# Kernel optimization log

Hardware: AMD Instinct MI355X
Metric: run time of the kernel (lower is better)

Reference implementation:

```python
import jax, jax.numpy as jnp
import numpy as np

DILATIONS = (1, 2, 4, 8)  # d1..d4 from init_kwargs
QUERY_C = 256
HEADS = 4


def setup_inputs() -> dict:
    key = jax.random.key(0)
    ks = jax.random.split(key, 7)
    b, c, h, w = 8, QUERY_C, 128, 128
    c4 = c // HEADS
    s1 = 1.0 / np.sqrt(c)          # kaiming-ish scale for 1x1 convs (fan_in=c)
    s3 = 1.0 / np.sqrt(c * 9)      # for 3x3 convs (fan_in=c*9)
    return {
        "query": jax.random.normal(ks[0], (b, c, h, w), dtype=jnp.float32),
        "Wq": jax.random.normal(ks[1], (HEADS, c4, c), dtype=jnp.float32) * s1,
        "bq": jax.random.normal(ks[2], (HEADS, c4), dtype=jnp.float32) * 0.01,
        "Wk": jax.random.normal(ks[3], (HEADS, c4, c, 3, 3), dtype=jnp.float32) * s3,
        "bk": jax.random.normal(ks[4], (HEADS, c4), dtype=jnp.float32) * 0.01,
        "Wv": jax.random.normal(ks[5], (HEADS, c4, c), dtype=jnp.float32) * s1,
        "bv": jax.random.normal(ks[6], (HEADS, c4), dtype=jnp.float32) * 0.01,
    }


def reference(query, Wq, bq, Wk, bk, Wv, bv):
    b, c, h, w = query.shape
    n = h * w
    c4 = c // HEADS
    xf = query.reshape(b, c, n)  # (b, c, N)

    # 1x1 conv projections for Q and V across all 4 heads at once.
    q = jnp.einsum('bcn,hoc->hbon', xf, Wq) + bq.swapaxes(0, 0)[:, None, :, None]  # (H,b,c4,N)
    v = jnp.einsum('bcn,hoc->hbon', xf, Wv) + bv[:, None, :, None]                  # (H,b,c4,N)

    # Dilated 3x3 key convs (dilation differs per head -> small fixed loop).
    keys = []
    for i, d in enumerate(DILATIONS):
        k = jax.lax.conv_general_dilated(
            query, Wk[i], window_strides=(1, 1),
            padding=[(d, d), (d, d)], rhs_dilation=(d, d),
            dimension_numbers=('NCHW', 'OIHW', 'NCHW'))
        keys.append(k.reshape(b, c4, n) + bk[i][None, :, None])
    k = jnp.stack(keys)  # (H, b, c4, N)

    # Channel attention: scores (H,b,c4,c4), contraction over N spatial tokens.
    scale = 1.0 / jnp.sqrt(jnp.asarray(c, dtype=query.dtype))
    scores = jnp.einsum('hbon,hbpn->hbop', q, k) * scale
    attn = jax.nn.softmax(scores, axis=-1)
    out = jnp.einsum('hbop,hbpn->hbon', attn, v)  # (H, b, c4, N)

    # torch: cat(split(out, 1, dim=0), dim=2).squeeze(0) -> heads concat on channel dim
    out = jnp.transpose(out, (1, 0, 2, 3)).reshape(b, c, h, w)
    return out
```

## Files before the change

kernel.cpp:

```cpp
#include <hip/hip_runtime.h>
#include <hip/hip_bf16.h>


typedef __attribute__((ext_vector_type(8))) _Float16 f16x8;
typedef __attribute__((ext_vector_type(4))) float f32x4;
typedef __attribute__((ext_vector_type(16))) float f32x16;

__device__ __forceinline__ unsigned short f2h(float f) {
  union { _Float16 h; unsigned short u; } v;
  v.h = (_Float16)f;
  return v.u;
}

__device__ __forceinline__ f32x4 mfma16(f16x8 a, f16x8 b, f32x4 c) {
  return __builtin_amdgcn_mfma_f32_16x16x32_f16(a, b, c, 0, 0, 0);
}
__device__ __forceinline__ f32x16 mfma32(f16x8 a, f16x8 b, f32x16 c) {
  return __builtin_amdgcn_mfma_f32_32x32x16_f16(a, b, c, 0, 0, 0);
}

__device__ __forceinline__ int sw(int row, int c) {
  return row * 64 + ((((c << 1) ^ ((row & 7) << 4)) >> 1));
}

__global__ __launch_bounds__(256) void prep(const float* __restrict__ Wq,
                                            const float* __restrict__ Wv,
                                            const float* __restrict__ Wk,
                                            unsigned short* __restrict__ Wqvn,
                                            unsigned short* __restrict__ Wkb,
                                            unsigned short* __restrict__ zp) {
  int i = blockIdx.x * 256 + threadIdx.x;
  if (blockIdx.x == 0) zp[threadIdx.x] = 0;
  const int total = 131072 + 589824;
  if (i >= total) return;
  if (i < 65536) {
    int jj = i & 7;
    int m31 = (i >> 3) & 31;
    int hi = (i >> 8) & 1;
    int ks = (i >> 9) & 15;
    int mt = i >> 13;
    int row = mt * 32 + m31;
    int ch = ks * 16 + hi * 8 + jj;
    Wqvn[i] = f2h(Wq[row * 256 + ch]);
  } else if (i < 131072) {
    int j2 = i - 65536;
    int p = j2 & 63;
    int c = (j2 >> 6) & 255;
    int h = j2 >> 14;
    Wqvn[i] = f2h(Wv[(size_t)(h * 64 + p) * 256 + c]);
  } else {
    int j = i - 131072;
    int jj = j & 7;
    int p = (j >> 3) & 63;
    int ks = (j >> 9) & 31;
    int ht = j >> 14;
    int t = ht % 9;
    int h = ht / 9;
    Wkb[j] = f2h(Wk[(size_t)((h * 64 + p) * 256 + ks * 8 + jj) * 9 + t]);
  }
}

__global__ __launch_bounds__(256) void xpose(const float* __restrict__ x,
                                             unsigned short* __restrict__ xT) {
  __shared__ unsigned short tile[64][66];
  int n0 = blockIdx.x * 64, c0 = blockIdx.y * 64, b = blockIdx.z;
  int t = threadIdx.x;
  int r = t >> 2, q = t & 3;
  const float* src = x + (size_t)b * 4194304 + (size_t)(c0 + r) * 16384 + n0 + q * 16;
#pragma unroll
  for (int i = 0; i < 4; i++) {
    float4 v = *(const float4*)(src + i * 4);
    tile[r][q * 16 + i * 4 + 0] = f2h(v.x);
    tile[r][q * 16 + i * 4 + 1] = f2h(v.y);
    tile[r][q * 16 + i * 4 + 2] = f2h(v.z);
    tile[r][q * 16 + i * 4 + 3] = f2h(v.w);
  }
  __syncthreads();
  int px = t & 63, s4 = t >> 6;
  unsigned short v[16];
#pragma unroll
  for (int j = 0; j < 16; j++) v[j] = tile[s4 * 16 + j][px];
  unsigned short* dst = xT + (size_t)b * 4194304 + (size_t)((c0 >> 4) + s4) * 262144 +
                        (size_t)(n0 + px) * 16;
  *(uint4*)&dst[0] = *(const uint4*)&v[0];
  *(uint4*)&dst[8] = *(const uint4*)&v[8];
}

__global__ __launch_bounds__(256) void proj(const unsigned short* __restrict__ xT,
                                            const unsigned short* __restrict__ Wqvn,
                                            const float* __restrict__ bq,
                                            unsigned short* __restrict__ qout) {
  __shared__ __align__(16) unsigned short Xs[2048 * 8];
  int n0 = blockIdx.x * 64, b = blockIdx.y;
  int tid = threadIdx.x, lane = tid & 63, w = tid >> 6;
  int l31 = lane & 31, hi = lane >> 5;
  const unsigned short* xb = xT + (size_t)b * 4194304;
#pragma unroll
  for (int it = 0; it < 8; it++) {
    int base = it * 256 + w * 64;
    int p = base + lane;
    int px = p >> 5, g = p & 31;
    int gs = g ^ (px & 31);
    const unsigned short* gsrc =
        xb + (size_t)(gs >> 1) * 262144 + (size_t)(n0 + px) * 16 + (gs & 1) * 8;
    __builtin_amdgcn_global_load_lds(
        (const __attribute__((address_space(1))) void*)gsrc,
        (__attribute__((address_space(3))) void*)&Xs[(size_t)base * 8], 16, 0, 0);
  }
  __syncthreads();

  f32x16 acc[2][2];
#pragma unroll
  for (int i = 0; i < 2; i++)
#pragma unroll
    for (int j = 0; j < 2; j++)
#pragma unroll
      for (int r = 0; r < 16; r++) acc[i][j][r] = 0.f;

#pragma unroll
  for (int ks = 0; ks < 16; ks++) {
    f16x8 bfr[2];
#pragma unroll
    for (int nt = 0; nt < 2; nt++) {
      int px = nt * 32 + l31;
      int gl = (ks * 2 + hi) ^ (px & 31);
      bfr[nt] = *(const f16x8*)&Xs[(px * 32 + gl) * 8];
    }
#pragma unroll
    for (int mj = 0; mj < 2; mj++) {
      int mt = w * 2 + mj;
      f16x8 afr = *(const f16x8*)(Wqvn + (size_t)(((mt * 16 + ks) * 2 + hi) * 32 + l31) * 8);
      acc[mj][0] = mfma32(afr, bfr[0], acc[mj][0]);
      acc[mj][1] = mfma32(afr, bfr[1], acc[mj][1]);
    }
  }

#pragma unroll
  for (int mj = 0; mj < 2; mj++) {
    int mt = w * 2 + mj;
#pragma unroll
    for (int nt = 0; nt < 2; nt++) {
      int n = n0 + nt * 32 + l31;
#pragma unroll
      for (int r = 0; r < 16; r++) {
        int og = mt * 32 + (r & 3) + 8 * (r >> 2) + 4 * hi;
        int h = og >> 6, o = og & 63;
        qout[((size_t)(h * 8 + b) * 64 + o) * 16384 + n] = f2h(acc[mj][nt][r] + bq[og]);
      }
    }
  }
}

__global__ __launch_bounds__(256, 2) void convk(const unsigned short* __restrict__ xT,
                                                const unsigned short* __restrict__ Wkb,
                                                const float* __restrict__ bk,
                                                const unsigned short* __restrict__ zp,
                                                unsigned short* __restrict__ kout) {
  __shared__ __align__(16) unsigned short Hs[2][1792 * 8];
  __shared__ __align__(16) unsigned short Ws[1280 * 8];
  int orig = (blockIdx.x & 7) * 128 + (blockIdx.x >> 3);
  int g = orig & 31, b = (orig >> 5) & 7, h = orig >> 8;
  int d = 1 << h;
  int gpd = 32 >> h;
  int s = g / gpd;
  int q0 = (g - s * gpd) * 4;
  int nq = 128 >> h;
  int tid = threadIdx.x, lane = tid & 63, w = tid >> 6;
  int l31 = lane & 31, hi = lane >> 5;
  const unsigned short* xb = xT + (size_t)b * 4194304;

  f32x16 acc[2][4];
#pragma unroll
  for (int i = 0; i < 2; i++)
#pragma unroll
    for (int j = 0; j < 4; j++)
#pragma unroll
      for (int r = 0; r < 16; r++) acc[i][j][r] = 0.f;

  const char* hptr[7];
  int hstr[7];
#pragma unroll
  for (int it = 0; it < 7; it++) {
    int p = it * 256 + tid;
    hptr[it] = (const char*)zp;
    hstr[it] = 0;
    if (p < 1728) {
      int px = p % 144;
      int sp = p / 144;
      int plane = sp % 6, slot = sp / 6;
      int q = q0 + plane - 1;
      int xc = px - d;
      bool ok = (q >= 0) & (q < nq) & (xc >= 0) & (xc < 128);
      if (ok) {
        hptr[it] = (const char*)(xb + (size_t)((s + q * d) * 128 + xc) * 16 + slot * 8);
        hstr[it] = 524288;
      }
    }
  }
  const char* wptr[5];
  int wstr[5];
#pragma unroll
  for (int it = 0; it < 5; it++) {
    int p = it * 256 + tid;
    wptr[it] = (const char*)zp;
    wstr[it] = 0;
    if (p < 1152) {
      int pp = p & 63, ts = p >> 6;
      int t = ts >> 1, slot = ts & 1;
      wptr[it] = (const char*)(Wkb + (size_t)(((h * 9 + t) * 32 + slot) * 64 + pp) * 8);
      wstr[it] = 2048;
    }
  }

  auto HSTAGE = [&](int bufi) {
#pragma unroll
    for (int it = 0; it < 7; it++) {
      int base = it * 256 + w * 64;
      __builtin_amdgcn_global_load_lds(
          (const __attribute__((address_space(1))) void*)hptr[it],
          (__attribute__((address_space(3))) void*)&Hs[bufi][(size_t)base * 8], 16, 0, 0);
      hptr[it] += hstr[it];
    }
  };
  auto WSTAGE = [&]() {
#pragma unroll
    for (int it = 0; it < 5; it++) {
      int base = it * 256 + w * 64;
      __builtin_amdgcn_global_load_lds(
          (const __attribute__((address_space(1))) void*)wptr[it],
          (__attribute__((address_space(3))) void*)&Ws[(size_t)base * 8], 16, 0, 0);
      wptr[it] += wstr[it];
    }
  };

  HSTAGE(0);
  WSTAGE();
  HSTAGE(1);
#pragma unroll 1
  for (int c = 0; c < 16; c++) {
    if (c < 15) asm volatile("s_waitcnt vmcnt(7)" ::: "memory");
    else        asm volatile("s_waitcnt vmcnt(0)" ::: "memory");
    __builtin_amdgcn_s_barrier();
    __builtin_amdgcn_sched_barrier(0);
    int bufi = c & 1;
    __builtin_amdgcn_s_setprio(1);
#pragma unroll
    for (int tx = 0; tx < 3; tx++) {
      f16x8 bfr[6];
#pragma unroll
      for (int p6 = 0; p6 < 6; p6++)
        bfr[p6] = *(const f16x8*)&Hs[bufi][((hi * 6 + p6) * 144 + w * 32 + d * tx + l31) * 8];
#pragma unroll
      for (int ty = 0; ty < 3; ty++) {
        int t = ty * 3 + tx;
        f16x8 a0 = *(const f16x8*)&Ws[((t * 2 + hi) * 64 + l31) * 8];
        f16x8 a1 = *(const f16x8*)&Ws[((t * 2 + hi) * 64 + 32 + l31) * 8];
#pragma unroll
        for (int r = 0; r < 4; r++) {
          acc[0][r] = mfma32(a0, bfr[r + ty], acc[0][r]);
          acc[1][r] = mfma32(a1, bfr[r + ty], acc[1][r]);
        }
      }
    }
    __builtin_amdgcn_s_setprio(0);
    asm volatile("s_waitcnt lgkmcnt(0)" ::: "memory");
    __builtin_amdgcn_sched_barrier(0);
    __builtin_amdgcn_s_barrier();
    __builtin_amdgcn_sched_barrier(0);
    if (c < 15) WSTAGE();
    if (c < 14) HSTAGE(bufi);
    __builtin_amdgcn_sched_barrier(0);
  }

  unsigned short* kb = kout + (size_t)((h * 8 + b) * 64) * 16384;
#pragma unroll
  for (int mo = 0; mo < 2; mo++)
#pragma unroll
    for (int r = 0; r < 4; r++) {
      int y = s + (q0 + r) * d;
#pragma unroll
      for (int reg = 0; reg < 16; reg++) {
        int p = mo * 32 + (reg & 3) + 8 * (reg >> 2) + 4 * hi;
        int x = w * 32 + l31;
        kb[(size_t)p * 16384 + y * 128 + x] = f2h(acc[mo][r][reg] + bk[h * 64 + p]);
      }
    }
}

__global__ __launch_bounds__(256) void scoresk(const unsigned short* __restrict__ qin,
                                               const unsigned short* __restrict__ kin,
                                               float* __restrict__ part) {
  __shared__ __align__(16) unsigned short As[64 * 64];
  __shared__ __align__(16) unsigned short Bs[64 * 64];
  int nch = blockIdx.x, b = blockIdx.y, h = blockIdx.z;
  int tid = threadIdx.x, lane = tid & 63, w = tid >> 6;
  int l15 = lane & 15, uq = lane >> 4;
  const unsigned short* qb = qin + (size_t)((h * 8 + b) * 64) * 16384;
  const unsigned short* kb = kin + (size_t)((h * 8 + b) * 64) * 16384;
  int moff = (w >> 1) * 32, noff = (w & 1) * 32;
  const f32x4 fz = {0.f, 0.f, 0.f, 0.f};
  f32x4 acc[2][2] = {{fz, fz}, {fz, fz}};
  const unsigned short* srcb = (w < 2) ? qb : kb;
  unsigned short* dst = (w < 2) ? As : Bs;
  int pbase = (w & 1) * 64;
  for (int ci = 0; ci < 8; ci++) {
    int nb = nch * 512 + ci * 64;
    __syncthreads();
#pragma unroll
    for (int k4 = 0; k4 < 4; k4++) {
      int p = pbase + k4 * 128 + lane;
      int row = p >> 3, j = p & 7;
      int gs = j ^ (row & 7);
      const unsigned short* gsrc = srcb + (size_t)row * 16384 + nb + gs * 8;
      __builtin_amdgcn_global_load_lds(
          (const __attribute__((address_space(1))) void*)gsrc,
          (__attribute__((address_space(3))) void*)&dst[(size_t)(pbase + k4 * 128) * 8],
          16, 0, 0);
    }
    asm volatile("s_waitcnt vmcnt(0)" ::: "memory");
    __syncthreads();
#pragma unroll
    for (int kk = 0; kk < 2; kk++) {
      f16x8 b0 = *(const f16x8*)&Bs[sw(noff + l15, kk * 32 + uq * 8)];
      f16x8 b1 = *(const f16x8*)&Bs[sw(noff + 16 + l15, kk * 32 + uq * 8)];
      f16x8 a0 = *(const f16x8*)&As[sw(moff + l15, kk * 32 + uq * 8)];
      f16x8 a1 = *(const f16x8*)&As[sw(moff + 16 + l15, kk * 32 + uq * 8)];
      acc[0][0] = mfma16(a0, b0, acc[0][0]);
      acc[0][1] = mfma16(a0, b1, acc[0][1]);
      acc[1][0] = mfma16(a1, b0, acc[1][0]);
      acc[1][1] = mfma16(a1, b1, acc[1][1]);
    }
  }
  float* pb = part + (size_t)((nch * 4 + h) * 8 + b) * 4096;
#pragma unroll
  for (int mf = 0; mf < 2; mf++)
#pragma unroll
    for (int nf = 0; nf < 2; nf++) {
      int p = noff + nf * 16 + l15;
#pragma unroll
      for (int r = 0; r < 4; r++) {
        int o = moff + mf * 16 + 4 * uq + r;
        pb[o * 64 + p] = acc[mf][nf][r];
      }
    }
}

__global__ __launch_bounds__(256) void smax(const float* __restrict__ part,
                                            const float* __restrict__ bv,
                                            unsigned short* __restrict__ attn,
                                            float* __restrict__ obias) {
  int row = blockIdx.x * 4 + (threadIdx.x >> 6);
  int lane = threadIdx.x & 63;
  int h = row >> 9, b = (row >> 6) & 7, o = row & 63;
  float s = 0.f;
#pragma unroll
  for (int nch = 0; nch < 32; nch++)
    s += part[(size_t)((nch * 4 + h) * 8 + b) * 4096 + o * 64 + lane];
  s *= 0.0625f;
  float m = s;
#pragma unroll
  for (int k = 32; k > 0; k >>= 1) m = fmaxf(m, __shfl_xor(m, k, 64));
  float e = __expf(s - m);
  float sum = e;
#pragma unroll
  for (int k = 32; k > 0; k >>= 1) sum += __shfl_xor(sum, k, 64);
  float a = e / sum;
  attn[(size_t)(h * 8 + b) * 4096 + o * 64 + lane] = f2h(a);
  float ob = a * bv[h * 64 + lane];
#pragma unroll
  for (int k = 32; k > 0; k >>= 1) ob += __shfl_xor(ob, k, 64);
  if (lane == 0) obias[b * 256 + h * 64 + o] = ob;
}

__global__ __launch_bounds__(256) void avP(const unsigned short* __restrict__ attn,
                                           const unsigned short* __restrict__ WvT,
                                           unsigned short* __restrict__ A2) {
  int b = blockIdx.x, h = blockIdx.y;
  int tid = threadIdx.x, lane = tid & 63, wq = tid >> 6;
  int l31 = lane & 31, hi = lane >> 5;
  const unsigned short* at = attn + (size_t)(h * 8 + b) * 4096;
  const unsigned short* wv = WvT + (size_t)h * 16384;
  f32x16 acc[2][2];
#pragma unroll
  for (int i = 0; i < 2; i++)
#pragma unroll
    for (int j = 0; j < 2; j++)
#pragma unroll
      for (int r = 0; r < 16; r++) acc[i][j][r] = 0.f;
#pragma unroll
  for (int ks = 0; ks < 4; ks++) {
    f16x8 a0 = *(const f16x8*)(at + (size_t)(l31)*64 + ks * 16 + hi * 8);
    f16x8 a1 = *(const f16x8*)(at + (size_t)(32 + l31) * 64 + ks * 16 + hi * 8);
    f16x8 b0 = *(const f16x8*)(wv + (size_t)(wq * 64 + l31) * 64 + ks * 16 + hi * 8);
    f16x8 b1 = *(const f16x8*)(wv + (size_t)(wq * 64 + 32 + l31) * 64 + ks * 16 + hi * 8);
    acc[0][0] = mfma32(a0, b0, acc[0][0]);
    acc[0][1] = mfma32(a0, b1, acc[0][1]);
    acc[1][0] = mfma32(a1, b0, acc[1][0]);
    acc[1][1] = mfma32(a1, b1, acc[1][1]);
  }
  unsigned short* a2b = A2 + (size_t)b * 65536;
#pragma unroll
  for (int mo = 0; mo < 2; mo++)
#pragma unroll
    for (int nf = 0; nf < 2; nf++)
#pragma unroll
      for (int r = 0; r < 16; r++) {
        int o = mo * 32 + (r & 3) + 8 * (r >> 2) + 4 * hi;
        int c = wq * 64 + nf * 32 + l31;
        a2b[(size_t)(h * 64 + o) * 256 + c] = f2h(acc[mo][nf][r]);
      }
}

__global__ __launch_bounds__(256) void outk2(const unsigned short* __restrict__ A2,
                                             const unsigned short* __restrict__ xT,
                                             const float* __restrict__ obias,
                                             float* __restrict__ out) {
  int n0 = blockIdx.x * 64, b = blockIdx.y;
  int tid = threadIdx.x, lane = tid & 63, w = tid >> 6;
  int l31 = lane & 31, hi = lane >> 5;
  const unsigned short* xb = xT + (size_t)b * 4194304;
  const unsigned short* a2b = A2 + (size_t)b * 65536;
  f32x16 acc[2][2];
#pragma unroll
  for (int i = 0; i < 2; i++)
#pragma unroll
    for (int j = 0; j < 2; j++)
#pragma unroll
      for (int r = 0; r < 16; r++) acc[i][j][r] = 0.f;
#pragma unroll
  for (int slab = 0; slab < 16; slab++) {
    f16x8 a0 = *(const f16x8*)(a2b + (size_t)(w * 64 + l31) * 256 + slab * 16 + hi * 8);
    f16x8 a1 = *(const f16x8*)(a2b + (size_t)(w * 64 + 32 + l31) * 256 + slab * 16 + hi * 8);
    f16x8 b0 = *(const f16x8*)(xb + (size_t)slab * 262144 + (size_t)(n0 + l31) * 16 + hi * 8);
    f16x8 b1 = *(const f16x8*)(xb + (size_t)slab * 262144 + (size_t)(n0 + 32 + l31) * 16 + hi * 8);
    acc[0][0] = mfma32(a0, b0, acc[0][0]);
    acc[0][1] = mfma32(a0, b1, acc[0][1]);
    acc[1][0] = mfma32(a1, b0, acc[1][0]);
    acc[1][1] = mfma32(a1, b1, acc[1][1]);
  }
  float* ob = out + (size_t)b * 4194304;
#pragma unroll
  for (int mo = 0; mo < 2; mo++)
#pragma unroll
    for (int nf = 0; nf < 2; nf++)
#pragma unroll
      for (int r = 0; r < 16; r++) {
        int oc = w * 64 + mo * 32 + (r & 3) + 8 * (r >> 2) + 4 * hi;
        int n = n0 + nf * 32 + l31;
        ob[(size_t)oc * 16384 + n] = acc[mo][nf][r] + obias[b * 256 + oc];
      }
}

extern "C" void kernel_launch(void* const* d_in, const int* in_sizes, int n_in,
                              void* d_out, int out_size, void* d_ws, size_t ws_size,
                              hipStream_t stream) {
  const float* x  = (const float*)d_in[0];
  const float* Wq = (const float*)d_in[1];
  const float* bq = (const float*)d_in[2];
  const float* Wk = (const float*)d_in[3];
  const float* bk = (const float*)d_in[4];
  const float* Wv = (const float*)d_in[5];
  const float* bv = (const float*)d_in[6];
  float* out = (float*)d_out;

  char* ws = (char*)d_ws;
  unsigned short* kbuf = (unsigned short*)(ws);
  unsigned short* A2   = (unsigned short*)(ws);
  float*          obias = (float*)(ws + 1048576);
  unsigned short* xT   = (unsigned short*)(ws + 67108864);
  unsigned short* attn = (unsigned short*)(ws + 134217728);
  unsigned short* Wqvn = (unsigned short*)(ws + 134479872);
  unsigned short* WvT  = (unsigned short*)(ws + 134610944);
  unsigned short* Wkb  = (unsigned short*)(ws + 134742016);
  unsigned short* zp   = (unsigned short*)(ws + 135921664);
  unsigned short* qb = (unsigned short*)d_out + 33554432;
  float* part = (float*)d_out;

  prep<<<dim3(2816), dim3(256), 0, stream>>>(Wq, Wv, Wk, Wqvn, Wkb, zp);
  xpose<<<dim3(256, 4, 8), dim3(256), 0, stream>>>(x, xT);
  proj<<<dim3(256, 8), dim3(256), 0, stream>>>(xT, Wqvn, bq, qb);
  convk<<<dim3(1024), dim3(256), 0, stream>>>(xT, Wkb, bk, zp, kbuf);
  scoresk<<<dim3(32, 8, 4), dim3(256), 0, stream>>>(qb, kbuf, part);
  smax<<<dim3(512), dim3(256), 0, stream>>>(part, bv, attn, obias);
  avP<<<dim3(8, 4), dim3(256), 0, stream>>>(attn, WvT, A2);
  outk2<<<dim3(256, 8), dim3(256), 0, stream>>>(A2, xT, obias, out);
}
```

Baseline: 321.3 us.

## Fuse QK score computation into key conv kernel, drop K buffer

The key convolution kernel now stages its biased fp16 output tile in LDS and immediately multiplies it against Q, writing per-block partial scores instead of storing K to global memory. The separate scores kernel is removed. The Q projection is rewritten to emit a fragment-friendly layout through an LDS transpose with 16-byte stores. This removes a full K write and readback plus a kernel launch, at the cost of extra LDS usage and an epilogue in the conv kernel, with Q read uncached from global inside the fused loop.

```diff
diff --git a/kernel.cpp b/kernel.cpp
--- a/kernel.cpp
+++ b/kernel.cpp
@@ -12,15 +12,8 @@
   return v.u;
 }
 
-__device__ __forceinline__ f32x4 mfma16(f16x8 a, f16x8 b, f32x4 c) {
-  return __builtin_amdgcn_mfma_f32_16x16x32_f16(a, b, c, 0, 0, 0);
-}
 __device__ __forceinline__ f32x16 mfma32(f16x8 a, f16x8 b, f32x16 c) {
   return __builtin_amdgcn_mfma_f32_32x32x16_f16(a, b, c, 0, 0, 0);
-}
-
-__device__ __forceinline__ int sw(int row, int c) {
-  return row * 64 + ((((c << 1) ^ ((row & 7) << 4)) >> 1));
 }
 
 __global__ __launch_bounds__(256) void prep(const float* __restrict__ Wq,
@@ -89,8 +82,9 @@
 __global__ __launch_bounds__(256) void proj(const unsigned short* __restrict__ xT,
                                             const unsigned short* __restrict__ Wqvn,
                                             const float* __restrict__ bq,
-                                            unsigned short* __restrict__ qout) {
+                                            unsigned short* __restrict__ qf) {
   __shared__ __align__(16) unsigned short Xs[2048 * 8];
+  __shared__ __align__(16) unsigned short Ls[64 * 264];
   int n0 = blockIdx.x * 64, b = blockIdx.y;
   int tid = threadIdx.x, lane = tid & 63, w = tid >> 6;
   int l31 = lane & 31, hi = lane >> 5;
@@ -140,14 +134,26 @@
     int mt = w * 2 + mj;
 #pragma unroll
     for (int nt = 0; nt < 2; nt++) {
-      int n = n0 + nt * 32 + l31;
+      int px = nt * 32 + l31;
 #pragma unroll
       for (int r = 0; r < 16; r++) {
         int og = mt * 32 + (r & 3) + 8 * (r >> 2) + 4 * hi;
-        int h = og >> 6, o = og & 63;
-        qout[((size_t)(h * 8 + b) * 64 + o) * 16384 + n] = f2h(acc[mj][nt][r] + bq[og]);
-      }
-    }
+        Ls[px * 264 + og] = f2h(acc[mj][nt][r] + bq[og]);
+      }
+    }
+  }
+  __syncthreads();
+#pragma unroll
+  for (int i = 0; i < 8; i++) {
+    int item = i * 256 + tid;
+    int og = item & 255, seg = item >> 8;
+    int h = og >> 6, o = og & 63;
+    unsigned short v[8];
+#pragma unroll
+    for (int j = 0; j < 8; j++) v[j] = Ls[(seg * 8 + j) * 264 + og];
+    size_t hb = (size_t)(h * 8 + b);
+    size_t nb16 = (size_t)(n0 >> 4) + (seg >> 1);
+    *(uint4*)&qf[((hb * 1024 + nb16) * 2 + (seg & 1)) * 512 + o * 8] = *(const uint4*)v;
   }
 }
 
@@ -155,9 +161,10 @@
                                                 const unsigned short* __restrict__ Wkb,
                                                 const float* __restrict__ bk,
                                                 const unsigned short* __restrict__ zp,
-                                                unsigned short* __restrict__ kout) {
-  __shared__ __align__(16) unsigned short Hs[2][1792 * 8];
-  __shared__ __align__(16) unsigned short Ws[1280 * 8];
+                                                const unsigned short* __restrict__ qf,
+                                                float* __restrict__ part) {
+  __shared__ __align__(16) unsigned short LDSB[38912];
+  unsigned short* Wsb = LDSB + 28672;
   int orig = (blockIdx.x & 7) * 128 + (blockIdx.x >> 3);
   int g = orig & 31, b = (orig >> 5) & 7, h = orig >> 8;
   int d = 1 << h;
@@ -213,12 +220,13 @@
   }
 
   auto HSTAGE = [&](int bufi) {
+    unsigned short* hb2 = LDSB + bufi * 14336;
 #pragma unroll
     for (int it = 0; it < 7; it++) {
       int base = it * 256 + w * 64;
       __builtin_amdgcn_global_load_lds(
           (const __attribute__((address_space(1))) void*)hptr[it],
-          (__attribute__((address_space(3))) void*)&Hs[bufi][(size_t)base * 8], 16, 0, 0);
+          (__attribute__((address_space(3))) void*)&hb2[(size_t)base * 8], 16, 0, 0);
       hptr[it] += hstr[it];
     }
   };
@@ -228,7 +236,7 @@
       int base = it * 256 + w * 64;
       __builtin_amdgcn_global_load_lds(
           (const __attribute__((address_space(1))) void*)wptr[it],
-          (__attribute__((address_space(3))) void*)&Ws[(size_t)base * 8], 16, 0, 0);
+          (__attribute__((address_space(3))) void*)&Wsb[(size_t)base * 8], 16, 0, 0);
       wptr[it] += wstr[it];
     }
   };
@@ -242,19 +250,19 @@
     else        asm volatile("s_waitcnt vmcnt(0)" ::: "memory");
     __builtin_amdgcn_s_barrier();
     __builtin_amdgcn_sched_barrier(0);
-    int bufi = c & 1;
+    const unsigned short* hb2 = LDSB + (c & 1) * 14336;
     __builtin_amdgcn_s_setprio(1);
 #pragma unroll
     for (int tx = 0; tx < 3; tx++) {
       f16x8 bfr[6];
 #pragma unroll
       for (int p6 = 0; p6 < 6; p6++)
-        bfr[p6] = *(const f16x8*)&Hs[bufi][((hi * 6 + p6) * 144 + w * 32 + d * tx + l31) * 8];
+        bfr[p6] = *(const f16x8*)&hb2[((hi * 6 + p6) * 144 + w * 32 + d * tx + l31) * 8];
 #pragma unroll
       for (int ty = 0; ty < 3; ty++) {
         int t = ty * 3 + tx;
-        f16x8 a0 = *(const f16x8*)&Ws[((t * 2 + hi) * 64 + l31) * 8];
-        f16x8 a1 = *(const f16x8*)&Ws[((t * 2 + hi) * 64 + 32 + l31) * 8];
+        f16x8 a0 = *(const f16x8*)&Wsb[((t * 2 + hi) * 64 + l31) * 8];
+        f16x8 a1 = *(const f16x8*)&Wsb[((t * 2 + hi) * 64 + 32 + l31) * 8];
 #pragma unroll
         for (int r = 0; r < 4; r++) {
           acc[0][r] = mfma32(a0, bfr[r + ty], acc[0][r]);
@@ -268,81 +276,44 @@
     __builtin_amdgcn_s_barrier();
     __builtin_amdgcn_sched_barrier(0);
     if (c < 15) WSTAGE();
-    if (c < 14) HSTAGE(bufi);
+    if (c < 14) HSTAGE(c & 1);
     __builtin_amdgcn_sched_barrier(0);
   }
 
-  unsigned short* kb = kout + (size_t)((h * 8 + b) * 64) * 16384;
+  __syncthreads();
+  unsigned short* Ks = LDSB;
 #pragma unroll
   for (int mo = 0; mo < 2; mo++)
 #pragma unroll
-    for (int r = 0; r < 4; r++) {
-      int y = s + (q0 + r) * d;
+    for (int r = 0; r < 4; r++)
 #pragma unroll
       for (int reg = 0; reg < 16; reg++) {
         int p = mo * 32 + (reg & 3) + 8 * (reg >> 2) + 4 * hi;
-        int x = w * 32 + l31;
-        kb[(size_t)p * 16384 + y * 128 + x] = f2h(acc[mo][r][reg] + bk[h * 64 + p]);
-      }
-    }
-}
-
-__global__ __launch_bounds__(256) void scoresk(const unsigned short* __restrict__ qin,
-                                               const unsigned short* __restrict__ kin,
-                                               float* __restrict__ part) {
-  __shared__ __align__(16) unsigned short As[64 * 64];
-  __shared__ __align__(16) unsigned short Bs[64 * 64];
-  int nch = blockIdx.x, b = blockIdx.y, h = blockIdx.z;
-  int tid = threadIdx.x, lane = tid & 63, w = tid >> 6;
-  int l15 = lane & 15, uq = lane >> 4;
-  const unsigned short* qb = qin + (size_t)((h * 8 + b) * 64) * 16384;
-  const unsigned short* kb = kin + (size_t)((h * 8 + b) * 64) * 16384;
-  int moff = (w >> 1) * 32, noff = (w & 1) * 32;
-  const f32x4 fz = {0.f, 0.f, 0.f, 0.f};
-  f32x4 acc[2][2] = {{fz, fz}, {fz, fz}};
-  const unsigned short* srcb = (w < 2) ? qb : kb;
-  unsigned short* dst = (w < 2) ? As : Bs;
-  int pbase = (w & 1) * 64;
-  for (int ci = 0; ci < 8; ci++) {
-    int nb = nch * 512 + ci * 64;
-    __syncthreads();
-#pragma unroll
-    for (int k4 = 0; k4 < 4; k4++) {
-      int p = pbase + k4 * 128 + lane;
-      int row = p >> 3, j = p & 7;
-      int gs = j ^ (row & 7);
-      const unsigned short* gsrc = srcb + (size_t)row * 16384 + nb + gs * 8;
-      __builtin_amdgcn_global_load_lds(
-          (const __attribute__((address_space(1))) void*)gsrc,
-          (__attribute__((address_space(3))) void*)&dst[(size_t)(pbase + k4 * 128) * 8],
-          16, 0, 0);
-    }
-    asm volatile("s_waitcnt vmcnt(0)" ::: "memory");
-    __syncthreads();
-#pragma unroll
-    for (int kk = 0; kk < 2; kk++) {
-      f16x8 b0 = *(const f16x8*)&Bs[sw(noff + l15, kk * 32 + uq * 8)];
-      f16x8 b1 = *(const f16x8*)&Bs[sw(noff + 16 + l15, kk * 32 + uq * 8)];
-      f16x8 a0 = *(const f16x8*)&As[sw(moff + l15, kk * 32 + uq * 8)];
-      f16x8 a1 = *(const f16x8*)&As[sw(moff + 16 + l15, kk * 32 + uq * 8)];
-      acc[0][0] = mfma16(a0, b0, acc[0][0]);
-      acc[0][1] = mfma16(a0, b1, acc[0][1]);
-      acc[1][0] = mfma16(a1, b0, acc[1][0]);
-      acc[1][1] = mfma16(a1, b1, acc[1][1]);
-    }
-  }
-  float* pb = part + (size_t)((nch * 4 + h) * 8 + b) * 4096;
-#pragma unroll
-  for (int mf = 0; mf < 2; mf++)
-#pragma unroll
-    for (int nf = 0; nf < 2; nf++) {
-      int p = noff + nf * 16 + l15;
-#pragma unroll
-      for (int r = 0; r < 4; r++) {
-        int o = moff + mf * 16 + 4 * uq + r;
-        pb[o * 64 + p] = acc[mf][nf][r];
-      }
-    }
+        int nl = r * 128 + w * 32 + l31;
+        Ks[p * 520 + nl] = f2h(acc[mo][r][reg] + bk[h * 64 + p]);
+      }
+  __syncthreads();
+  int o0 = (w & 1) * 32, p0 = (w >> 1) * 32;
+  f32x16 sacc;
+#pragma unroll
+  for (int r = 0; r < 16; r++) sacc[r] = 0.f;
+  const unsigned short* qfb = qf + (size_t)(h * 8 + b) * 1048576;
+#pragma unroll
+  for (int ks = 0; ks < 32; ks++) {
+    int r = ks >> 3;
+    int x0 = (ks & 7) * 16;
+    int y = s + (q0 + r) * d;
+    size_t nb16 = (size_t)(y * 8) + (x0 >> 4);
+    f16x8 aq = *(const f16x8*)(qfb + (nb16 * 2 + hi) * 512 + (o0 + l31) * 8);
+    f16x8 bk2 = *(const f16x8*)&Ks[(p0 + l31) * 520 + ks * 16 + hi * 8];
+    sacc = mfma32(aq, bk2, sacc);
+  }
+  float* pb = part + (size_t)((g * 4 + h) * 8 + b) * 4096;
+#pragma unroll
+  for (int reg = 0; reg < 16; reg++) {
+    int o = o0 + (reg & 3) + 8 * (reg >> 2) + 4 * hi;
+    pb[o * 64 + p0 + l31] = sacc[reg];
+  }
 }
 
 __global__ __launch_bounds__(256) void smax(const float* __restrict__ part,
@@ -464,7 +435,6 @@
   float* out = (float*)d_out;
 
   char* ws = (char*)d_ws;
-  unsigned short* kbuf = (unsigned short*)(ws);
   unsigned short* A2   = (unsigned short*)(ws);
   float*          obias = (float*)(ws + 1048576);
   unsigned short* xT   = (unsigned short*)(ws + 67108864);
@@ -473,14 +443,13 @@
   unsigned short* WvT  = (unsigned short*)(ws + 134610944);
   unsigned short* Wkb  = (unsigned short*)(ws + 134742016);
   unsigned short* zp   = (unsigned short*)(ws + 135921664);
-  unsigned short* qb = (unsigned short*)d_out + 33554432;
+  unsigned short* qf = (unsigned short*)d_out + 33554432;
   float* part = (float*)d_out;
 
   prep<<<dim3(2816), dim3(256), 0, stream>>>(Wq, Wv, Wk, Wqvn, Wkb, zp);
   xpose<<<dim3(256, 4, 8), dim3(256), 0, stream>>>(x, xT);
-  proj<<<dim3(256, 8), dim3(256), 0, stream>>>(xT, Wqvn, bq, qb);
-  convk<<<dim3(1024), dim3(256), 0, stream>>>(xT, Wkb, bk, zp, kbuf);
-  scoresk<<<dim3(32, 8, 4), dim3(256), 0, stream>>>(qb, kbuf, part);
+  proj<<<dim3(256, 8), dim3(256), 0, stream>>>(xT, Wqvn, bq, qf);
+  convk<<<dim3(1024), dim3(256), 0, stream>>>(xT, Wkb, bk, zp, qf, part);
   smax<<<dim3(512), dim3(256), 0, stream>>>(part, bv, attn, obias);
   avP<<<dim3(8, 4), dim3(256), 0, stream>>>(attn, WvT, A2);
   outk2<<<dim3(256, 8), dim3(256), 0, stream>>>(A2, xT, obias, out);
```

After: 290.5 us. -9.6%, faster.
